# Kernel tuning notes

Hardware: AMD Instinct MI355X
Metric: run time of the kernel (lower is better)

Reference implementation:

```python
import jax, jax.numpy as jnp
import numpy as np

LOG_2PI = float(np.log(2.0 * np.pi))
NUM_STATES, NUM_TYPES, NUM_GENES, NUM_SAMPLES = 32, 128, 8192, 8192


def setup_inputs() -> dict:
    key = jax.random.key(0)
    k1, k2, k3, k4, k5 = jax.random.split(key, 5)
    cell_prob = jax.random.uniform(k1, (NUM_STATES, NUM_TYPES), dtype=jnp.float32)
    cell_prob = cell_prob / cell_prob.sum(axis=1, keepdims=True)  # rows on simplex
    Z_mu = jax.random.normal(k2, (NUM_TYPES, NUM_GENES), dtype=jnp.float32)
    Z_sigma = jax.random.uniform(k3, (NUM_TYPES, NUM_GENES), dtype=jnp.float32) + 0.1
    X = jax.random.normal(k4, (NUM_SAMPLES, NUM_GENES), dtype=jnp.float32)
    day = jax.random.randint(k5, (NUM_SAMPLES,), 1, NUM_STATES + 1)  # 1-based days
    return {"cell_prob": cell_prob, "Z_mu": Z_mu, "Z_sigma": Z_sigma, "X": X, "day": day}


def reference(cell_prob, Z_mu, Z_sigma, X, day):
    # mu[st, g] = sum_t cell_prob[st,t] * Z_mu[t,g]
    mu = jnp.matmul(cell_prob, Z_mu)                        # (states, genes)
    sigma = jnp.matmul(cell_prob ** 2, Z_sigma)             # (states, genes)
    # cov term: original double loop sums a_i * a_j over i<j where
    # a_t[st,g] = cell_prob[st,t] * Z_sigma[t,g]; use 2*sum_{i<j} = (sum)^2 - sum^2
    A = cell_prob[:, :, None] * Z_sigma[None, :, :]          # (states, types, genes)
    sigma = sigma + (A.sum(axis=1) ** 2 - (A ** 2).sum(axis=1))
    # dayToState: state = day - min_days (min_days = 1); shift=False -> S = 0
    state = day - 1                                          # (samples,)
    mu_s = mu[state]                                         # (samples, genes)
    sg_s = sigma[state]                                      # (samples, genes)
    # Normal(mu, sigma).log_prob(X): sigma is used as the scale, as in torch
    z = (X - mu_s) / sg_s
    logp = -0.5 * z * z - jnp.log(sg_s) - 0.5 * LOG_2PI      # (samples, genes)
    return logp.sum(), logp
```

## Files before the change

kernel.cpp:

```cpp
#include <hip/hip_runtime.h>
#include <math.h>

#define N_STATES 32
#define N_TYPES 128
#define N_GENES 8192
#define N_SAMPLES 8192
#define LOG2PI_F 1.8378770664093453f

typedef float f32x4 __attribute__((ext_vector_type(4)));

__global__ __launch_bounds__(256) void precompute_kernel(
    const float* __restrict__ cp, const float* __restrict__ Zmu,
    const float* __restrict__ Zs, float* __restrict__ muT,
    float* __restrict__ invT) {
  __shared__ float s_cp[N_TYPES], s_cp2[N_TYPES];
  const int st = blockIdx.y;
  const int g0 = blockIdx.x * 1024 + threadIdx.x * 4;

  if (threadIdx.x < N_TYPES) {
    float c = cp[st * N_TYPES + threadIdx.x];
    s_cp[threadIdx.x] = c;
    s_cp2[threadIdx.x] = c * c;
  }
  __syncthreads();

  float mu[4] = {0,0,0,0}, s13[4] = {0,0,0,0}, s2[4] = {0,0,0,0};
#pragma unroll 1
  for (int t = 0; t < N_TYPES; t += 4) {
    f32x4 zm[4], zs[4];
#pragma unroll
    for (int u = 0; u < 4; ++u) {
      zm[u] = *(const f32x4*)(Zmu + (size_t)(t + u) * N_GENES + g0);
      zs[u] = *(const f32x4*)(Zs  + (size_t)(t + u) * N_GENES + g0);
    }
#pragma unroll
    for (int u = 0; u < 4; ++u) {
      float c = s_cp[t + u], c2 = s_cp2[t + u];
#pragma unroll
      for (int j = 0; j < 4; ++j) {
        mu[j]  = fmaf(c, zm[u][j], mu[j]);
        s2[j]  = fmaf(c, zs[u][j], s2[j]);
        s13[j] = fmaf(c2, zs[u][j] * (1.f - zs[u][j]), s13[j]);
      }
    }
  }

  f32x4 mv, iv;
#pragma unroll
  for (int j = 0; j < 4; ++j) {
    float sigma = s13[j] + s2[j] * s2[j];
    mv[j] = mu[j];
    iv[j] = 1.0f / sigma;
  }
  int o = st * N_GENES + g0;
  *(f32x4*)(muT + o)  = mv;
  *(f32x4*)(invT + o) = iv;
}

__global__ __launch_bounds__(256) void main_kernel(
    const float* __restrict__ X, const int* __restrict__ day,
    const float* __restrict__ muT, const float* __restrict__ invT,
    float* __restrict__ out, float* __restrict__ partial) {
  const int row0 = blockIdx.x * 4;
  const int tid = threadIdx.x;
  float acc = 0.f;

#pragma unroll 1
  for (int r = 0; r < 4; ++r) {
    const int row = row0 + r;
    const int st = day[row] - 1;
    const f32x4* Xr = (const f32x4*)(X + (size_t)row * N_GENES) + tid;
    const f32x4* Mr = (const f32x4*)(muT + (size_t)st * N_GENES) + tid;
    const f32x4* Ir = (const f32x4*)(invT + (size_t)st * N_GENES) + tid;

    f32x4 x[8], m[8], iv[8];
#pragma unroll
    for (int it = 0; it < 8; ++it) x[it]  = Xr[it * 256];
#pragma unroll
    for (int it = 0; it < 8; ++it) m[it]  = Mr[it * 256];
#pragma unroll
    for (int it = 0; it < 8; ++it) iv[it] = Ir[it * 256];
    __builtin_amdgcn_sched_barrier(0);

    float* ob = out + (size_t)row * N_GENES + 1 + tid * 4;
#pragma unroll
    for (int it = 0; it < 8; ++it) {
      f32x4 p;
#pragma unroll
      for (int j = 0; j < 4; ++j) {
        float z = (x[it][j] - m[it][j]) * iv[it][j];
        p[j] = fmaf(-0.5f * z, z, __logf(iv[it][j]) - 0.5f * LOG2PI_F);
      }
      float* o4 = ob + it * 1024;
      __builtin_nontemporal_store(p[0], o4 + 0);
      __builtin_nontemporal_store(p[1], o4 + 1);
      __builtin_nontemporal_store(p[2], o4 + 2);
      __builtin_nontemporal_store(p[3], o4 + 3);
      acc += (p[0] + p[1]) + (p[2] + p[3]);
    }
  }

#pragma unroll
  for (int off = 32; off; off >>= 1) acc += __shfl_down(acc, off, 64);
  __shared__ float s_w[4];
  int lane = threadIdx.x & 63, w = threadIdx.x >> 6;
  if (lane == 0) s_w[w] = acc;
  __syncthreads();
  if (threadIdx.x == 0)
    partial[blockIdx.x] = (s_w[0] + s_w[1]) + (s_w[2] + s_w[3]);
}

__global__ __launch_bounds__(256) void reduce_kernel(
    const float* __restrict__ partial, int n, float* __restrict__ out0) {
  double acc = 0.0;
  for (int i = threadIdx.x; i < n; i += 256) acc += (double)partial[i];
#pragma unroll
  for (int off = 32; off; off >>= 1) acc += __shfl_down(acc, off, 64);
  __shared__ double s_w[4];
  int lane = threadIdx.x & 63, w = threadIdx.x >> 6;
  if (lane == 0) s_w[w] = acc;
  __syncthreads();
  if (threadIdx.x == 0) out0[0] = (float)((s_w[0] + s_w[1]) + (s_w[2] + s_w[3]));
}

extern "C" void kernel_launch(void* const* d_in, const int* in_sizes, int n_in,
                              void* d_out, int out_size, void* d_ws, size_t ws_size,
                              hipStream_t stream) {
  const float* cp  = (const float*)d_in[0];
  const float* Zmu = (const float*)d_in[1];
  const float* Zs  = (const float*)d_in[2];
  const float* X   = (const float*)d_in[3];
  const int*   day = (const int*)d_in[4];
  float* out = (float*)d_out;
  float* ws  = (float*)d_ws;

  const int TBL = N_STATES * N_GENES;
  float* muT     = ws;
  float* invT    = ws + TBL;
  float* partial = ws + 2 * TBL;

  dim3 g1(N_GENES / 1024, N_STATES);
  precompute_kernel<<<g1, 256, 0, stream>>>(cp, Zmu, Zs, muT, invT);

  const int NBLK = N_SAMPLES / 4;
  main_kernel<<<NBLK, 256, 0, stream>>>(X, day, muT, invT, out, partial);
  reduce_kernel<<<1, 256, 0, stream>>>(partial, NBLK, out);
}
```

Before: 135.1 us.

## Pack mu and inverse sigma as bf16 pairs and double-buffer row loads

The precompute kernel now writes one table of packed bf16 mu and bf16 1/sigma per gene instead of two fp32 tables. This halves table traffic in the main kernel. The main kernel also software-pipelines its four rows with two register buffers so the loads for the next row are in flight while the current row is computed, and it writes output with inline-asm dwordx4 stores instead of scalar nontemporal stores. The risk is a loss of precision in mu and 1/sigma, which may exceed the output tolerance, plus higher register pressure.

```diff
diff --git a/kernel.cpp b/kernel.cpp
--- a/kernel.cpp
+++ b/kernel.cpp
@@ -8,11 +8,16 @@
 #define LOG2PI_F 1.8378770664093453f
 
 typedef float f32x4 __attribute__((ext_vector_type(4)));
+typedef unsigned int u32x4 __attribute__((ext_vector_type(4)));
+
+__device__ __forceinline__ unsigned int bf16r(float f) {
+  unsigned int u = __builtin_bit_cast(unsigned int, f);
+  return (u + 0x7FFFu + ((u >> 16) & 1u)) >> 16;
+}
 
 __global__ __launch_bounds__(256) void precompute_kernel(
     const float* __restrict__ cp, const float* __restrict__ Zmu,
-    const float* __restrict__ Zs, float* __restrict__ muT,
-    float* __restrict__ invT) {
+    const float* __restrict__ Zs, unsigned int* __restrict__ T) {
   __shared__ float s_cp[N_TYPES], s_cp2[N_TYPES];
   const int st = blockIdx.y;
   const int g0 = blockIdx.x * 1024 + threadIdx.x * 4;
@@ -45,60 +50,73 @@
     }
   }
 
-  f32x4 mv, iv;
+  u32x4 pk;
 #pragma unroll
   for (int j = 0; j < 4; ++j) {
     float sigma = s13[j] + s2[j] * s2[j];
-    mv[j] = mu[j];
-    iv[j] = 1.0f / sigma;
+    pk[j] = (bf16r(mu[j]) << 16) | bf16r(1.0f / sigma);
   }
-  int o = st * N_GENES + g0;
-  *(f32x4*)(muT + o)  = mv;
-  *(f32x4*)(invT + o) = iv;
+  *(u32x4*)(T + (size_t)st * N_GENES + g0) = pk;
+}
+
+__device__ __forceinline__ void issue_row(const float* __restrict__ Xr,
+                                          const unsigned int* __restrict__ Tr,
+                                          int tid, f32x4 (&xb)[8], u32x4 (&tb)[8]) {
+  const f32x4* Xp = (const f32x4*)Xr + tid;
+  const u32x4* Tp = (const u32x4*)Tr + tid;
+#pragma unroll
+  for (int it = 0; it < 8; ++it) xb[it] = Xp[it * 256];
+#pragma unroll
+  for (int it = 0; it < 8; ++it) tb[it] = Tp[it * 256];
+  __builtin_amdgcn_sched_barrier(0x6);
+}
+
+__device__ __forceinline__ float compute_row(float* __restrict__ outr,
+                                             const f32x4 (&xb)[8],
+                                             const u32x4 (&tb)[8]) {
+  float acc = 0.f;
+#pragma unroll
+  for (int it = 0; it < 8; ++it) {
+    f32x4 p;
+#pragma unroll
+    for (int j = 0; j < 4; ++j) {
+      unsigned int tv = tb[it][j];
+      float mu = __builtin_bit_cast(float, tv & 0xFFFF0000u);
+      float iv = __builtin_bit_cast(float, tv << 16);
+      float z = (xb[it][j] - mu) * iv;
+      p[j] = fmaf(-0.5f * z, z, __logf(iv) - 0.5f * LOG2PI_F);
+    }
+    float* oa = outr + it * 1024;
+    asm volatile("global_store_dwordx4 %0, %1, off" : : "v"(oa), "v"(p) : "memory");
+    acc += (p[0] + p[1]) + (p[2] + p[3]);
+  }
+  return acc;
 }
 
 __global__ __launch_bounds__(256) void main_kernel(
     const float* __restrict__ X, const int* __restrict__ day,
-    const float* __restrict__ muT, const float* __restrict__ invT,
-    float* __restrict__ out, float* __restrict__ partial) {
+    const unsigned int* __restrict__ T, float* __restrict__ out,
+    float* __restrict__ partial) {
   const int row0 = blockIdx.x * 4;
   const int tid = threadIdx.x;
+
+  const int st0 = day[row0] - 1, st1 = day[row0 + 1] - 1;
+  const int st2 = day[row0 + 2] - 1, st3 = day[row0 + 3] - 1;
+  const float* Xb = X + (size_t)row0 * N_GENES;
+  float* ob = out + (size_t)row0 * N_GENES + 1 + tid * 4;
+
+  f32x4 xa[8], xc[8];
+  u32x4 ta[8], tc[8];
   float acc = 0.f;
 
-#pragma unroll 1
-  for (int r = 0; r < 4; ++r) {
-    const int row = row0 + r;
-    const int st = day[row] - 1;
-    const f32x4* Xr = (const f32x4*)(X + (size_t)row * N_GENES) + tid;
-    const f32x4* Mr = (const f32x4*)(muT + (size_t)st * N_GENES) + tid;
-    const f32x4* Ir = (const f32x4*)(invT + (size_t)st * N_GENES) + tid;
-
-    f32x4 x[8], m[8], iv[8];
-#pragma unroll
-    for (int it = 0; it < 8; ++it) x[it]  = Xr[it * 256];
-#pragma unroll
-    for (int it = 0; it < 8; ++it) m[it]  = Mr[it * 256];
-#pragma unroll
-    for (int it = 0; it < 8; ++it) iv[it] = Ir[it * 256];
-    __builtin_amdgcn_sched_barrier(0);
-
-    float* ob = out + (size_t)row * N_GENES + 1 + tid * 4;
-#pragma unroll
-    for (int it = 0; it < 8; ++it) {
-      f32x4 p;
-#pragma unroll
-      for (int j = 0; j < 4; ++j) {
-        float z = (x[it][j] - m[it][j]) * iv[it][j];
-        p[j] = fmaf(-0.5f * z, z, __logf(iv[it][j]) - 0.5f * LOG2PI_F);
-      }
-      float* o4 = ob + it * 1024;
-      __builtin_nontemporal_store(p[0], o4 + 0);
-      __builtin_nontemporal_store(p[1], o4 + 1);
-      __builtin_nontemporal_store(p[2], o4 + 2);
-      __builtin_nontemporal_store(p[3], o4 + 3);
-      acc += (p[0] + p[1]) + (p[2] + p[3]);
-    }
-  }
+  issue_row(Xb,               T + (size_t)st0 * N_GENES, tid, xa, ta);
+  issue_row(Xb + N_GENES,     T + (size_t)st1 * N_GENES, tid, xc, tc);
+  acc += compute_row(ob, xa, ta);
+  issue_row(Xb + 2 * N_GENES, T + (size_t)st2 * N_GENES, tid, xa, ta);
+  acc += compute_row(ob + N_GENES, xc, tc);
+  issue_row(Xb + 3 * N_GENES, T + (size_t)st3 * N_GENES, tid, xc, tc);
+  acc += compute_row(ob + 2 * N_GENES, xa, ta);
+  acc += compute_row(ob + 3 * N_GENES, xc, tc);
 
 #pragma unroll
   for (int off = 32; off; off >>= 1) acc += __shfl_down(acc, off, 64);
@@ -135,14 +153,13 @@
   float* ws  = (float*)d_ws;
 
   const int TBL = N_STATES * N_GENES;
-  float* muT     = ws;
-  float* invT    = ws + TBL;
-  float* partial = ws + 2 * TBL;
+  unsigned int* T = (unsigned int*)ws;
+  float* partial  = ws + TBL;
 
   dim3 g1(N_GENES / 1024, N_STATES);
-  precompute_kernel<<<g1, 256, 0, stream>>>(cp, Zmu, Zs, muT, invT);
+  precompute_kernel<<<g1, 256, 0, stream>>>(cp, Zmu, Zs, T);
 
   const int NBLK = N_SAMPLES / 4;
-  main_kernel<<<NBLK, 256, 0, stream>>>(X, day, muT, invT, out, partial);
+  main_kernel<<<NBLK, 256, 0, stream>>>(X, day, T, out, partial);
   reduce_kernel<<<1, 256, 0, stream>>>(partial, NBLK, out);
 }
```

Measured after the change: 159.3 us. 17.9% more time.
